# Optimization experiments

Hardware: AMD Instinct MI355X
Metric: run time of the kernel (lower is better)

## Reference

```python
import jax, jax.numpy as jnp
import numpy as np

NENV, SEQ, LATENT = 4096, 128, 64
EMB, HID = 256, 1024
SA = 2  # state_action_size


def setup_inputs() -> dict:
    key = jax.random.key(0)
    ks = jax.random.split(key, 8)
    def w(k, shape):
        return (jax.random.normal(k, shape, jnp.float32) / np.sqrt(shape[0])).astype(jnp.float32)
    return {
        "z": jax.random.normal(ks[0], (NENV, SEQ, LATENT), jnp.float32),
        "rnn_hxs": jnp.zeros((NENV, HID), jnp.float32),
        "w1": w(ks[1], (SA + LATENT, 32)), "b1": jnp.zeros((32,), jnp.float32),
        "w2": w(ks[2], (32, EMB)),          "b2": jnp.zeros((EMB,), jnp.float32),
        "wih": w(ks[3], (EMB, 3 * HID)),    "bih": jnp.zeros((3 * HID,), jnp.float32),
        "whh": w(ks[4], (HID, 3 * HID)),    "bhh": jnp.zeros((3 * HID,), jnp.float32),
        "w3": w(ks[5], (HID, HID // 2)),    "b3": jnp.zeros((HID // 2,), jnp.float32),
        "w4": w(ks[6], (HID // 2, SA)),     "b4": jnp.zeros((SA,), jnp.float32),
    }


def _gru_cell(x, h, wih, whh, bih, bhh):
    # PyTorch nn.GRU single-step semantics.
    gi = x @ wih + bih                    # [n, 3H]
    gh = h @ whh + bhh                    # [n, 3H]
    i_r, i_z, i_n = jnp.split(gi, 3, axis=-1)
    h_r, h_z, h_n = jnp.split(gh, 3, axis=-1)
    r = jax.nn.sigmoid(i_r + h_r)
    u = jax.nn.sigmoid(i_z + h_z)
    n = jnp.tanh(i_n + r * h_n)
    return (1.0 - u) * n + u * h


def reference(z, rnn_hxs, w1, b1, w2, b2, wih, bih, whh, bhh, w3, b3, w4, b4):
    zt = jnp.transpose(z, (1, 0, 2))                     # [S, N, latent]
    state0 = -2.0 * jnp.ones((z.shape[0], SA), z.dtype)  # initial fake action/state

    def step(carry, z_t):
        state, h = carry
        x = jnp.concatenate([state, z_t], axis=-1)       # [N, 2+latent]
        x = jax.nn.relu(x @ w1 + b1)
        x = jax.nn.relu(x @ w2 + b2)                     # mlp_in -> [N, EMB]
        h = _gru_cell(x, h, wih, whh, bih, bhh)          # [N, HID]
        o = jax.nn.relu(h @ w3 + b3)
        o = jnp.tanh(o @ w4 + b4)                        # output_linear -> [N, 2]
        return (o, h), o

    (_, h_new), outs = jax.lax.scan(step, (state0, rnn_hxs), zt)
    # original returns outputs.permute(1,0,2) -> [nenv, seq, 2], plus new hidden
    return jnp.transpose(outs, (1, 0, 2)), h_new
```

## Files before the change

kernel.cpp:

```cpp
#include <hip/hip_runtime.h>
#include <cstdint>
#include <cstddef>

#define NENV 4096
#define SEQ  128
#define LATENT 64
#define EMB  256
#define HID  1024
#define SA   2

typedef _Float16 half8 __attribute__((ext_vector_type(8)));
typedef float f32x4 __attribute__((ext_vector_type(4)));

__device__ __forceinline__ float sigmoid_f(float x){ return 1.0f/(1.0f + __expf(-x)); }

__global__ void transpose_cvt_kernel(const float* __restrict__ in, _Float16* __restrict__ out,
                                     int K, int C){
  int n = K*C;
  for (int i = blockIdx.x*blockDim.x + threadIdx.x; i < n; i += gridDim.x*blockDim.x){
    int c = i / K;
    int k = i - c*K;
    out[i] = (_Float16)in[(size_t)k*C + c];
  }
}

__global__ void init_h_kernel(const float* __restrict__ rnn, float* __restrict__ h32,
                              _Float16* __restrict__ h16){
  int n = NENV*HID;
  for (int i = blockIdx.x*blockDim.x + threadIdx.x; i < n; i += gridDim.x*blockDim.x){
    float v = rnn[i];
    h32[i] = v;
    h16[i] = (_Float16)v;
  }
}

__device__ __forceinline__ void gru_kloop(
    const _Float16* __restrict__ A, const _Float16* __restrict__ W, int K,
    int r0, int c0, int arow, int aseg, int m, int q, int n0,
    _Float16* As, _Float16* Ws0, _Float16* Ws1, _Float16* Ws2,
    f32x4* acc_r, f32x4* acc_z, f32x4* accn)
{
  for (int k0 = 0; k0 < K; k0 += 32){
    half8 la  = *(const half8*)(A + (size_t)(r0 + arow)*K + k0 + aseg*8);
    half8 lw0 = *(const half8*)(W + (size_t)(          c0 + arow)*K + k0 + aseg*8);
    half8 lw1 = *(const half8*)(W + (size_t)(HID     + c0 + arow)*K + k0 + aseg*8);
    half8 lw2 = *(const half8*)(W + (size_t)(2*HID   + c0 + arow)*K + k0 + aseg*8);
    __syncthreads();
    *(half8*)&As [arow*40 + aseg*8] = la;
    *(half8*)&Ws0[arow*40 + aseg*8] = lw0;
    *(half8*)&Ws1[arow*40 + aseg*8] = lw1;
    *(half8*)&Ws2[arow*40 + aseg*8] = lw2;
    __syncthreads();
    half8 br = *(const half8*)&Ws0[(n0+m)*40 + q*8];
    half8 bz = *(const half8*)&Ws1[(n0+m)*40 + q*8];
    half8 bn = *(const half8*)&Ws2[(n0+m)*40 + q*8];
#pragma unroll
    for (int mt = 0; mt < 4; ++mt){
      half8 a = *(const half8*)&As[(mt*16 + m)*40 + q*8];
      acc_r[mt] = __builtin_amdgcn_mfma_f32_16x16x32_f16(a, br, acc_r[mt], 0, 0, 0);
      acc_z[mt] = __builtin_amdgcn_mfma_f32_16x16x32_f16(a, bz, acc_z[mt], 0, 0, 0);
      accn[mt]  = __builtin_amdgcn_mfma_f32_16x16x32_f16(a, bn, accn[mt], 0, 0, 0);
    }
  }
}

__global__ __launch_bounds__(256, 4) void gru_kernel(
    const _Float16* __restrict__ x2h, const _Float16* __restrict__ hcur16,
    const _Float16* __restrict__ wihT, const _Float16* __restrict__ whhT,
    const float* __restrict__ bih, const float* __restrict__ bhh,
    float* __restrict__ h32, _Float16* __restrict__ hnxt16)
{
  __shared__ _Float16 As[64*40];
  __shared__ _Float16 Ws0[64*40];
  __shared__ _Float16 Ws1[64*40];
  __shared__ _Float16 Ws2[64*40];
  const int r0 = blockIdx.x*64, c0 = blockIdx.y*64;
  const int tid = threadIdx.x;
  const int lane = tid & 63, wave = tid >> 6;
  const int m = lane & 15, q = lane >> 4, n0 = wave*16;
  const int arow = tid >> 2, aseg = tid & 3;

  f32x4 zero4 = {0.f, 0.f, 0.f, 0.f};
  f32x4 acc_r[4], acc_z[4], acc_in[4], acc_hn[4];
#pragma unroll
  for (int i = 0; i < 4; ++i){ acc_r[i]=zero4; acc_z[i]=zero4; acc_in[i]=zero4; acc_hn[i]=zero4; }

  gru_kloop(x2h,    wihT, EMB, r0, c0, arow, aseg, m, q, n0, As, Ws0, Ws1, Ws2, acc_r, acc_z, acc_in);
  gru_kloop(hcur16, whhT, HID, r0, c0, arow, aseg, m, q, n0, As, Ws0, Ws1, Ws2, acc_r, acc_z, acc_hn);

  const int gc = c0 + n0 + m;
  float b_r  = bih[gc]         + bhh[gc];
  float b_z  = bih[gc + HID]   + bhh[gc + HID];
  float b_in = bih[gc + 2*HID];
  float b_hn = bhh[gc + 2*HID];
#pragma unroll
  for (int mt = 0; mt < 4; ++mt){
#pragma unroll
    for (int r = 0; r < 4; ++r){
      int grow = r0 + mt*16 + q*4 + r;
      float rr = sigmoid_f(acc_r[mt][r] + b_r);
      float u  = sigmoid_f(acc_z[mt][r] + b_z);
      float nn = tanhf(acc_in[mt][r] + b_in + rr*(acc_hn[mt][r] + b_hn));
      size_t idx = (size_t)grow*HID + gc;
      float hold = h32[idx];
      float hnew = (1.0f - u)*nn + u*hold;
      h32[idx] = hnew;
      hnxt16[idx] = (_Float16)hnew;
    }
  }
}

__global__ __launch_bounds__(256, 4) void out1_kernel(
    const _Float16* __restrict__ h16, const _Float16* __restrict__ w3T,
    const float* __restrict__ b3, float* __restrict__ o1)
{
  __shared__ _Float16 As[64*40];
  __shared__ _Float16 Ws[64*40];
  const int r0 = blockIdx.x*64, c0 = blockIdx.y*64;
  const int tid = threadIdx.x;
  const int lane = tid & 63, wave = tid >> 6;
  const int m = lane & 15, q = lane >> 4, n0 = wave*16;
  const int arow = tid >> 2, aseg = tid & 3;

  f32x4 zero4 = {0.f, 0.f, 0.f, 0.f};
  f32x4 acc[4];
#pragma unroll
  for (int i = 0; i < 4; ++i) acc[i] = zero4;

  for (int k0 = 0; k0 < HID; k0 += 32){
    half8 la = *(const half8*)(h16 + (size_t)(r0 + arow)*HID + k0 + aseg*8);
    half8 lw = *(const half8*)(w3T + (size_t)(c0 + arow)*HID + k0 + aseg*8);
    __syncthreads();
    *(half8*)&As[arow*40 + aseg*8] = la;
    *(half8*)&Ws[arow*40 + aseg*8] = lw;
    __syncthreads();
    half8 b = *(const half8*)&Ws[(n0+m)*40 + q*8];
#pragma unroll
    for (int mt = 0; mt < 4; ++mt){
      half8 a = *(const half8*)&As[(mt*16 + m)*40 + q*8];
      acc[mt] = __builtin_amdgcn_mfma_f32_16x16x32_f16(a, b, acc[mt], 0, 0, 0);
    }
  }
  const int gc = c0 + n0 + m;
  float bb = b3[gc];
#pragma unroll
  for (int mt = 0; mt < 4; ++mt){
#pragma unroll
    for (int r = 0; r < 4; ++r){
      int grow = r0 + mt*16 + q*4 + r;
      o1[(size_t)grow*(HID/2) + gc] = fmaxf(acc[mt][r] + bb, 0.f);
    }
  }
}

__global__ void tail_head_kernel(
    const float* __restrict__ o1, const float* __restrict__ w4, const float* __restrict__ b4,
    const float* __restrict__ z,  const float* __restrict__ w1, const float* __restrict__ b1,
    const float* __restrict__ w2, const float* __restrict__ b2,
    _Float16* __restrict__ x2h, float* __restrict__ out, int t, int mode)
{
  __shared__ float sw2[32*256];
  __shared__ float sw1[66*32];
  __shared__ float sz[16][64];
  __shared__ float sx1[16][32];
  __shared__ float sst[16][2];
  const int tid = threadIdx.x;
  const int r0 = blockIdx.x*16;

  if (mode != 2){
    for (int i = tid; i < 66*32; i += 256) sw1[i] = w1[i];
    for (int i = tid; i < 32*256; i += 256) sw2[i] = w2[i];
    int zt = (mode == 0) ? 0 : (t + 1);
    for (int i = tid; i < 16*64; i += 256){
      int r = i >> 6, k = i & 63;
      sz[r][k] = z[(size_t)(r0 + r)*SEQ*LATENT + zt*LATENT + k];
    }
  }

  if (mode != 0){
    int r = tid >> 4, p = tid & 15;
    const float* orow = o1 + (size_t)(r0 + r)*(HID/2);
    float a0 = 0.f, a1 = 0.f;
    for (int k = p*32; k < p*32 + 32; ++k){
      float v = orow[k];
      a0 += v*w4[k*2];
      a1 += v*w4[k*2 + 1];
    }
#pragma unroll
    for (int off = 1; off < 16; off <<= 1){
      a0 += __shfl_xor(a0, off);
      a1 += __shfl_xor(a1, off);
    }
    if (p == 0){
      a0 = tanhf(a0 + b4[0]);
      a1 = tanhf(a1 + b4[1]);
      out[(size_t)(r0 + r)*SEQ*SA + t*SA + 0] = a0;
      out[(size_t)(r0 + r)*SEQ*SA + t*SA + 1] = a1;
      sst[r][0] = a0; sst[r][1] = a1;
    }
  } else {
    if (tid < 32) sst[tid >> 1][tid & 1] = -2.0f;
  }
  __syncthreads();

  if (mode != 2){
    for (int it = tid; it < 16*32; it += 256){
      int r = it >> 5, j = it & 31;
      float acc = b1[j];
      acc += sst[r][0]*sw1[0*32 + j] + sst[r][1]*sw1[1*32 + j];
#pragma unroll 8
      for (int k = 0; k < 64; ++k) acc += sz[r][k]*sw1[(k + 2)*32 + j];
      sx1[r][j] = fmaxf(acc, 0.f);
    }
    __syncthreads();
    int col = tid;
    for (int r = 0; r < 16; ++r){
      float acc = b2[col];
#pragma unroll
      for (int k = 0; k < 32; ++k) acc += sx1[r][k]*sw2[k*256 + col];
      x2h[(size_t)(r0 + r)*EMB + col] = (_Float16)fmaxf(acc, 0.f);
    }
  }
}

extern "C" void kernel_launch(void* const* d_in, const int* in_sizes, int n_in,
                              void* d_out, int out_size, void* d_ws, size_t ws_size,
                              hipStream_t stream) {
  const float* z   = (const float*)d_in[0];
  const float* rnn = (const float*)d_in[1];
  const float* w1  = (const float*)d_in[2];
  const float* b1  = (const float*)d_in[3];
  const float* w2  = (const float*)d_in[4];
  const float* b2  = (const float*)d_in[5];
  const float* wih = (const float*)d_in[6];
  const float* bih = (const float*)d_in[7];
  const float* whh = (const float*)d_in[8];
  const float* bhh = (const float*)d_in[9];
  const float* w3  = (const float*)d_in[10];
  const float* b3  = (const float*)d_in[11];
  const float* w4  = (const float*)d_in[12];
  const float* b4  = (const float*)d_in[13];
  float* out = (float*)d_out;

  char* ws = (char*)d_ws;
  _Float16* wihT = (_Float16*)ws;                 ws += (size_t)3*HID*EMB*2;
  _Float16* whhT = (_Float16*)ws;                 ws += (size_t)3*HID*HID*2;
  _Float16* w3T  = (_Float16*)ws;                 ws += (size_t)(HID/2)*HID*2;
  _Float16* h16a = (_Float16*)ws;                 ws += (size_t)NENV*HID*2;
  _Float16* h16b = (_Float16*)ws;                 ws += (size_t)NENV*HID*2;
  float*    h32  = (float*)ws;                    ws += (size_t)NENV*HID*4;
  _Float16* x2h  = (_Float16*)ws;                 ws += (size_t)NENV*EMB*2;
  float*    o1   = (float*)ws;                    ws += (size_t)NENV*(HID/2)*4;

  transpose_cvt_kernel<<<512, 256, 0, stream>>>(wih, wihT, EMB, 3*HID);
  transpose_cvt_kernel<<<1024, 256, 0, stream>>>(whh, whhT, HID, 3*HID);
  transpose_cvt_kernel<<<256, 256, 0, stream>>>(w3, w3T, HID, HID/2);
  init_h_kernel<<<1024, 256, 0, stream>>>(rnn, h32, h16a);

  tail_head_kernel<<<NENV/16, 256, 0, stream>>>(o1, w4, b4, z, w1, b1, w2, b2, x2h, out, 0, 0);

  for (int t = 0; t < SEQ; ++t){
    _Float16* hc = (t & 1) ? h16b : h16a;
    _Float16* hn = (t & 1) ? h16a : h16b;
    gru_kernel<<<dim3(NENV/64, HID/64), 256, 0, stream>>>(x2h, hc, wihT, whhT, bih, bhh, h32, hn);
    out1_kernel<<<dim3(NENV/64, (HID/2)/64), 256, 0, stream>>>(hn, w3T, b3, o1);
    tail_head_kernel<<<NENV/16, 256, 0, stream>>>(o1, w4, b4, z, w1, b1, w2, b2, x2h, out,
                                                  t, (t < SEQ - 1) ? 1 : 2);
  }

  hipMemcpyAsync(out + (size_t)NENV*SEQ*SA, h32, (size_t)NENV*HID*sizeof(float),
                 hipMemcpyDeviceToDevice, stream);
}
```

Baseline: 11.20 ms.

## Retile GRU and output GEMMs to 128-row tiles with 32x32 MFMA and direct LDS loads

The GRU and out1 GEMM kernels now use 128x64 block tiles, 32x32x16 MFMA instructions, and global_load_lds DMA that writes straight into shared memory instead of going through registers. Block indices are remapped so neighbouring column groups land on the same XCD, which is meant to improve L2 reuse of weights. The o1 intermediate is stored in fp16 to halve its traffic. Together these aim to raise MFMA utilization and cut global and LDS traffic. The cost is fewer resident blocks per CU, an unpadded LDS layout that may cause bank conflicts, and reduced precision for o1.

Result: slower. 13.35 ms (+19.2%).

```diff
diff --git a/kernel.cpp b/kernel.cpp
--- a/kernel.cpp
+++ b/kernel.cpp
@@ -10,9 +10,19 @@
 #define SA   2
 
 typedef _Float16 half8 __attribute__((ext_vector_type(8)));
-typedef float f32x4 __attribute__((ext_vector_type(4)));
+typedef float f32x16 __attribute__((ext_vector_type(16)));
 
 __device__ __forceinline__ float sigmoid_f(float x){ return 1.0f/(1.0f + __expf(-x)); }
+
+__device__ __forceinline__ void dma16(const void* g, void* l){
+  __builtin_amdgcn_global_load_lds(
+      (const __attribute__((address_space(1))) void*)g,
+      (__attribute__((address_space(3))) void*)l, 16, 0, 0);
+}
+
+__device__ __forceinline__ f32x16 mfma32(half8 a, half8 b, f32x16 c){
+  return __builtin_amdgcn_mfma_f32_32x32x16_f16(a, b, c, 0, 0, 0);
+}
 
 __global__ void transpose_cvt_kernel(const float* __restrict__ in, _Float16* __restrict__ out,
                                      int K, int C){
@@ -34,127 +44,162 @@
   }
 }
 
-__device__ __forceinline__ void gru_kloop(
-    const _Float16* __restrict__ A, const _Float16* __restrict__ W, int K,
-    int r0, int c0, int arow, int aseg, int m, int q, int n0,
-    _Float16* As, _Float16* Ws0, _Float16* Ws1, _Float16* Ws2,
-    f32x4* acc_r, f32x4* acc_z, f32x4* accn)
+__device__ __forceinline__ void gru_phase(
+    const _Float16* __restrict__ Ap, const _Float16* __restrict__ Wp, int K,
+    int r0, int c0, int tid, int wave, int lane, int rbase, int cbase,
+    half8* smem, f32x16* accR, f32x16* accZ, f32x16* accN)
 {
+  const int l31 = lane & 31, lhi = lane >> 5;
+  const _Float16* g0; const _Float16* g1; const _Float16* g2; const _Float16* g3; const _Float16* g4;
+  { int slot = tid;        int kc = slot >> 7, row = slot & 127;
+    g0 = Ap + (size_t)(r0 + row)*K + kc*8; }
+  { int slot = 256 + tid;  int kc = slot >> 7, row = slot & 127;
+    g1 = Ap + (size_t)(r0 + row)*K + kc*8; }
+  { int s2 = tid;          int gate = s2 >> 8, kc = (s2 >> 6) & 3, col = s2 & 63;
+    g2 = Wp + (size_t)(gate*HID + c0 + col)*K + kc*8; }
+  { int s2 = 256 + tid;    int gate = s2 >> 8, kc = (s2 >> 6) & 3, col = s2 & 63;
+    g3 = Wp + (size_t)(gate*HID + c0 + col)*K + kc*8; }
+  { int s2 = 512 + tid;    int gate = s2 >> 8, kc = (s2 >> 6) & 3, col = s2 & 63;
+    g4 = Wp + (size_t)(gate*HID + c0 + col)*K + kc*8; }
+  char* lbase = (char*)smem;
+  char* l0 = lbase + (size_t)(0*256 + wave*64)*16;
+  char* l1 = lbase + (size_t)(1*256 + wave*64)*16;
+  char* l2 = lbase + (size_t)(2*256 + wave*64)*16;
+  char* l3 = lbase + (size_t)(3*256 + wave*64)*16;
+  char* l4 = lbase + (size_t)(4*256 + wave*64)*16;
+
   for (int k0 = 0; k0 < K; k0 += 32){
-    half8 la  = *(const half8*)(A + (size_t)(r0 + arow)*K + k0 + aseg*8);
-    half8 lw0 = *(const half8*)(W + (size_t)(          c0 + arow)*K + k0 + aseg*8);
-    half8 lw1 = *(const half8*)(W + (size_t)(HID     + c0 + arow)*K + k0 + aseg*8);
-    half8 lw2 = *(const half8*)(W + (size_t)(2*HID   + c0 + arow)*K + k0 + aseg*8);
-    __syncthreads();
-    *(half8*)&As [arow*40 + aseg*8] = la;
-    *(half8*)&Ws0[arow*40 + aseg*8] = lw0;
-    *(half8*)&Ws1[arow*40 + aseg*8] = lw1;
-    *(half8*)&Ws2[arow*40 + aseg*8] = lw2;
-    __syncthreads();
-    half8 br = *(const half8*)&Ws0[(n0+m)*40 + q*8];
-    half8 bz = *(const half8*)&Ws1[(n0+m)*40 + q*8];
-    half8 bn = *(const half8*)&Ws2[(n0+m)*40 + q*8];
-#pragma unroll
-    for (int mt = 0; mt < 4; ++mt){
-      half8 a = *(const half8*)&As[(mt*16 + m)*40 + q*8];
-      acc_r[mt] = __builtin_amdgcn_mfma_f32_16x16x32_f16(a, br, acc_r[mt], 0, 0, 0);
-      acc_z[mt] = __builtin_amdgcn_mfma_f32_16x16x32_f16(a, bz, acc_z[mt], 0, 0, 0);
-      accn[mt]  = __builtin_amdgcn_mfma_f32_16x16x32_f16(a, bn, accn[mt], 0, 0, 0);
-    }
-  }
-}
-
-__global__ __launch_bounds__(256, 4) void gru_kernel(
-    const _Float16* __restrict__ x2h, const _Float16* __restrict__ hcur16,
+    dma16(g0, l0); dma16(g1, l1); dma16(g2, l2); dma16(g3, l3); dma16(g4, l4);
+    g0 += 32; g1 += 32; g2 += 32; g3 += 32; g4 += 32;
+    __syncthreads();
+#pragma unroll
+    for (int c = 0; c < 2; ++c){
+      const int kc = c*2 + lhi;
+      half8 a0 = smem[kc*128 + rbase      + l31];
+      half8 a1 = smem[kc*128 + rbase + 32 + l31];
+      half8 b0 = smem[512 +        kc*64 + cbase + l31];
+      half8 b1 = smem[512 + 256 +  kc*64 + cbase + l31];
+      half8 b2 = smem[512 + 512 +  kc*64 + cbase + l31];
+      accR[0] = mfma32(a0, b0, accR[0]);
+      accR[1] = mfma32(a1, b0, accR[1]);
+      accZ[0] = mfma32(a0, b1, accZ[0]);
+      accZ[1] = mfma32(a1, b1, accZ[1]);
+      accN[0] = mfma32(a0, b2, accN[0]);
+      accN[1] = mfma32(a1, b2, accN[1]);
+    }
+    __syncthreads();
+  }
+}
+
+__global__ __launch_bounds__(256, 2) void gru_kernel(
+    const _Float16* __restrict__ x2h, const _Float16* __restrict__ hcur,
     const _Float16* __restrict__ wihT, const _Float16* __restrict__ whhT,
     const float* __restrict__ bih, const float* __restrict__ bhh,
-    float* __restrict__ h32, _Float16* __restrict__ hnxt16)
+    float* __restrict__ h32, _Float16* __restrict__ hnxt)
 {
-  __shared__ _Float16 As[64*40];
-  __shared__ _Float16 Ws0[64*40];
-  __shared__ _Float16 Ws1[64*40];
-  __shared__ _Float16 Ws2[64*40];
-  const int r0 = blockIdx.x*64, c0 = blockIdx.y*64;
+  __shared__ half8 smem[1280];
   const int tid = threadIdx.x;
   const int lane = tid & 63, wave = tid >> 6;
-  const int m = lane & 15, q = lane >> 4, n0 = wave*16;
-  const int arow = tid >> 2, aseg = tid & 3;
-
-  f32x4 zero4 = {0.f, 0.f, 0.f, 0.f};
-  f32x4 acc_r[4], acc_z[4], acc_in[4], acc_hn[4];
-#pragma unroll
-  for (int i = 0; i < 4; ++i){ acc_r[i]=zero4; acc_z[i]=zero4; acc_in[i]=zero4; acc_hn[i]=zero4; }
-
-  gru_kloop(x2h,    wihT, EMB, r0, c0, arow, aseg, m, q, n0, As, Ws0, Ws1, Ws2, acc_r, acc_z, acc_in);
-  gru_kloop(hcur16, whhT, HID, r0, c0, arow, aseg, m, q, n0, As, Ws0, Ws1, Ws2, acc_r, acc_z, acc_hn);
-
-  const int gc = c0 + n0 + m;
-  float b_r  = bih[gc]         + bhh[gc];
-  float b_z  = bih[gc + HID]   + bhh[gc + HID];
-  float b_in = bih[gc + 2*HID];
-  float b_hn = bhh[gc + 2*HID];
-#pragma unroll
-  for (int mt = 0; mt < 4; ++mt){
-#pragma unroll
-    for (int r = 0; r < 4; ++r){
-      int grow = r0 + mt*16 + q*4 + r;
-      float rr = sigmoid_f(acc_r[mt][r] + b_r);
-      float u  = sigmoid_f(acc_z[mt][r] + b_z);
-      float nn = tanhf(acc_in[mt][r] + b_in + rr*(acc_hn[mt][r] + b_hn));
-      size_t idx = (size_t)grow*HID + gc;
+  const int id = blockIdx.x;
+  const int xcd = id & 7, slot = id >> 3;
+  const int colg = xcd*2 + (slot & 1);
+  const int rowg = slot >> 1;
+  const int r0 = rowg*128, c0 = colg*64;
+  const int rbase = (wave & 1)*64, cbase = (wave >> 1)*32;
+  const int l31 = lane & 31, lhi = lane >> 5;
+
+  f32x16 accR[2], accZ[2], accN1[2], accN2[2];
+#pragma unroll
+  for (int i = 0; i < 16; ++i){
+    accR[0][i]=0.f; accR[1][i]=0.f; accZ[0][i]=0.f; accZ[1][i]=0.f;
+    accN1[0][i]=0.f; accN1[1][i]=0.f; accN2[0][i]=0.f; accN2[1][i]=0.f;
+  }
+
+  gru_phase(x2h,  wihT, EMB, r0, c0, tid, wave, lane, rbase, cbase, smem, accR, accZ, accN1);
+  gru_phase(hcur, whhT, HID, r0, c0, tid, wave, lane, rbase, cbase, smem, accR, accZ, accN2);
+
+  const int gc = c0 + cbase + l31;
+  const float b_r  = bih[gc]         + bhh[gc];
+  const float b_z  = bih[gc + HID]   + bhh[gc + HID];
+  const float b_in = bih[gc + 2*HID];
+  const float b_hn = bhh[gc + 2*HID];
+#pragma unroll
+  for (int rt = 0; rt < 2; ++rt){
+#pragma unroll
+    for (int reg = 0; reg < 16; ++reg){
+      int row = r0 + rbase + rt*32 + (reg & 3) + 8*(reg >> 2) + 4*lhi;
+      float rr = sigmoid_f(accR[rt][reg] + b_r);
+      float u  = sigmoid_f(accZ[rt][reg] + b_z);
+      float nn = tanhf(accN1[rt][reg] + b_in + rr*(accN2[rt][reg] + b_hn));
+      size_t idx = (size_t)row*HID + gc;
       float hold = h32[idx];
       float hnew = (1.0f - u)*nn + u*hold;
       h32[idx] = hnew;
-      hnxt16[idx] = (_Float16)hnew;
-    }
-  }
-}
-
-__global__ __launch_bounds__(256, 4) void out1_kernel(
+      hnxt[idx] = (_Float16)hnew;
+    }
+  }
+}
+
+__global__ __launch_bounds__(256, 2) void out1_kernel(
     const _Float16* __restrict__ h16, const _Float16* __restrict__ w3T,
-    const float* __restrict__ b3, float* __restrict__ o1)
+    const float* __restrict__ b3, _Float16* __restrict__ o1)
 {
-  __shared__ _Float16 As[64*40];
-  __shared__ _Float16 Ws[64*40];
-  const int r0 = blockIdx.x*64, c0 = blockIdx.y*64;
+  __shared__ half8 smem[768];
   const int tid = threadIdx.x;
   const int lane = tid & 63, wave = tid >> 6;
-  const int m = lane & 15, q = lane >> 4, n0 = wave*16;
-  const int arow = tid >> 2, aseg = tid & 3;
-
-  f32x4 zero4 = {0.f, 0.f, 0.f, 0.f};
-  f32x4 acc[4];
-#pragma unroll
-  for (int i = 0; i < 4; ++i) acc[i] = zero4;
+  const int id = blockIdx.x;
+  const int colg = id & 7;
+  const int rowg = id >> 3;
+  const int r0 = rowg*128, c0 = colg*64;
+  const int rbase = (wave & 1)*64, cbase = (wave >> 1)*32;
+  const int l31 = lane & 31, lhi = lane >> 5;
+
+  f32x16 acc[2];
+#pragma unroll
+  for (int i = 0; i < 16; ++i){ acc[0][i]=0.f; acc[1][i]=0.f; }
+
+  const _Float16* g0; const _Float16* g1; const _Float16* g2;
+  { int slot = tid;       int kc = slot >> 7, row = slot & 127;
+    g0 = h16 + (size_t)(r0 + row)*HID + kc*8; }
+  { int slot = 256 + tid; int kc = slot >> 7, row = slot & 127;
+    g1 = h16 + (size_t)(r0 + row)*HID + kc*8; }
+  { int kc = tid >> 6, col = tid & 63;
+    g2 = w3T + (size_t)(c0 + col)*HID + kc*8; }
+  char* lbase = (char*)smem;
+  char* l0 = lbase + (size_t)(0*256 + wave*64)*16;
+  char* l1 = lbase + (size_t)(1*256 + wave*64)*16;
+  char* l2 = lbase + (size_t)(2*256 + wave*64)*16;
 
   for (int k0 = 0; k0 < HID; k0 += 32){
-    half8 la = *(const half8*)(h16 + (size_t)(r0 + arow)*HID + k0 + aseg*8);
-    half8 lw = *(const half8*)(w3T + (size_t)(c0 + arow)*HID + k0 + aseg*8);
-    __syncthreads();
-    *(half8*)&As[arow*40 + aseg*8] = la;
-    *(half8*)&Ws[arow*40 + aseg*8] = lw;
-    __syncthreads();
-    half8 b = *(const half8*)&Ws[(n0+m)*40 + q*8];
-#pragma unroll
-    for (int mt = 0; mt < 4; ++mt){
-      half8 a = *(const half8*)&As[(mt*16 + m)*40 + q*8];
-      acc[mt] = __builtin_amdgcn_mfma_f32_16x16x32_f16(a, b, acc[mt], 0, 0, 0);
-    }
-  }
-  const int gc = c0 + n0 + m;
-  float bb = b3[gc];
-#pragma unroll
-  for (int mt = 0; mt < 4; ++mt){
-#pragma unroll
-    for (int r = 0; r < 4; ++r){
-      int grow = r0 + mt*16 + q*4 + r;
-      o1[(size_t)grow*(HID/2) + gc] = fmaxf(acc[mt][r] + bb, 0.f);
+    dma16(g0, l0); dma16(g1, l1); dma16(g2, l2);
+    g0 += 32; g1 += 32; g2 += 32;
+    __syncthreads();
+#pragma unroll
+    for (int c = 0; c < 2; ++c){
+      const int kc = c*2 + lhi;
+      half8 a0 = smem[kc*128 + rbase      + l31];
+      half8 a1 = smem[kc*128 + rbase + 32 + l31];
+      half8 b  = smem[512 + kc*64 + cbase + l31];
+      acc[0] = mfma32(a0, b, acc[0]);
+      acc[1] = mfma32(a1, b, acc[1]);
+    }
+    __syncthreads();
+  }
+
+  const int gc = c0 + cbase + l31;
+  const float bb = b3[gc];
+#pragma unroll
+  for (int rt = 0; rt < 2; ++rt){
+#pragma unroll
+    for (int reg = 0; reg < 16; ++reg){
+      int row = r0 + rbase + rt*32 + (reg & 3) + 8*(reg >> 2) + 4*lhi;
+      o1[(size_t)row*(HID/2) + gc] = (_Float16)fmaxf(acc[rt][reg] + bb, 0.f);
     }
   }
 }
 
 __global__ void tail_head_kernel(
-    const float* __restrict__ o1, const float* __restrict__ w4, const float* __restrict__ b4,
+    const _Float16* __restrict__ o1, const float* __restrict__ w4, const float* __restrict__ b4,
     const float* __restrict__ z,  const float* __restrict__ w1, const float* __restrict__ b1,
     const float* __restrict__ w2, const float* __restrict__ b2,
     _Float16* __restrict__ x2h, float* __restrict__ out, int t, int mode)
@@ -179,10 +224,10 @@
 
   if (mode != 0){
     int r = tid >> 4, p = tid & 15;
-    const float* orow = o1 + (size_t)(r0 + r)*(HID/2);
+    const _Float16* orow = o1 + (size_t)(r0 + r)*(HID/2);
     float a0 = 0.f, a1 = 0.f;
     for (int k = p*32; k < p*32 + 32; ++k){
-      float v = orow[k];
+      float v = (float)orow[k];
       a0 += v*w4[k*2];
       a1 += v*w4[k*2 + 1];
     }
@@ -250,7 +295,7 @@
   _Float16* h16b = (_Float16*)ws;                 ws += (size_t)NENV*HID*2;
   float*    h32  = (float*)ws;                    ws += (size_t)NENV*HID*4;
   _Float16* x2h  = (_Float16*)ws;                 ws += (size_t)NENV*EMB*2;
-  float*    o1   = (float*)ws;                    ws += (size_t)NENV*(HID/2)*4;
+  _Float16* o1   = (_Float16*)ws;                 ws += (size_t)NENV*(HID/2)*2;
 
   transpose_cvt_kernel<<<512, 256, 0, stream>>>(wih, wihT, EMB, 3*HID);
   transpose_cvt_kernel<<<1024, 256, 0, stream>>>(whh, whhT, HID, 3*HID);
@@ -262,8 +307,8 @@
   for (int t = 0; t < SEQ; ++t){
     _Float16* hc = (t & 1) ? h16b : h16a;
     _Float16* hn = (t & 1) ? h16a : h16b;
-    gru_kernel<<<dim3(NENV/64, HID/64), 256, 0, stream>>>(x2h, hc, wihT, whhT, bih, bhh, h32, hn);
-    out1_kernel<<<dim3(NENV/64, (HID/2)/64), 256, 0, stream>>>(hn, w3T, b3, o1);
+    gru_kernel<<<512, 256, 0, stream>>>(x2h, hc, wihT, whhT, bih, bhh, h32, hn);
+    out1_kernel<<<256, 256, 0, stream>>>(hn, w3T, b3, o1);
     tail_head_kernel<<<NENV/16, 256, 0, stream>>>(o1, w4, b4, z, w1, b1, w2, b2, x2h, out,
                                                   t, (t < SEQ - 1) ? 1 : 2);
   }
```

## Use direct global-to-LDS loads, drop fp32 hidden state, fp16 intermediate output

Applied to the files above, without the earlier changes.

The GEMM kernels now stage tiles through global_load_lds DMA straight into unpadded LDS instead of going through registers. The fp32 hidden-state copy is removed: the recurrence reads the old h from the fp16 buffer and writes fp32 only on the final step, and the o1 activations are stored as fp16. Block ids are remapped so that neighbouring blocks share weight column groups. Together these cut global traffic and register staging, but carrying h in fp16 across 128 steps may hurt accuracy, and the unpadded LDS layout may cause bank conflicts.

Result: faster. 10.90 ms (-2.7%).

```diff
diff --git a/kernel.cpp b/kernel.cpp
--- a/kernel.cpp
+++ b/kernel.cpp
@@ -13,6 +13,16 @@
 typedef float f32x4 __attribute__((ext_vector_type(4)));
 
 __device__ __forceinline__ float sigmoid_f(float x){ return 1.0f/(1.0f + __expf(-x)); }
+
+__device__ __forceinline__ void dma16(const void* g, void* l){
+  __builtin_amdgcn_global_load_lds(
+      (const __attribute__((address_space(1))) void*)g,
+      (__attribute__((address_space(3))) void*)l, 16, 0, 0);
+}
+
+__device__ __forceinline__ f32x4 mfma16(half8 a, half8 b, f32x4 c){
+  return __builtin_amdgcn_mfma_f32_16x16x32_f16(a, b, c, 0, 0, 0);
+}
 
 __global__ void transpose_cvt_kernel(const float* __restrict__ in, _Float16* __restrict__ out,
                                      int K, int C){
@@ -24,137 +34,149 @@
   }
 }
 
-__global__ void init_h_kernel(const float* __restrict__ rnn, float* __restrict__ h32,
-                              _Float16* __restrict__ h16){
+__global__ void init_h_kernel(const float* __restrict__ rnn, _Float16* __restrict__ h16){
   int n = NENV*HID;
   for (int i = blockIdx.x*blockDim.x + threadIdx.x; i < n; i += gridDim.x*blockDim.x){
-    float v = rnn[i];
-    h32[i] = v;
-    h16[i] = (_Float16)v;
-  }
-}
-
-__device__ __forceinline__ void gru_kloop(
-    const _Float16* __restrict__ A, const _Float16* __restrict__ W, int K,
-    int r0, int c0, int arow, int aseg, int m, int q, int n0,
-    _Float16* As, _Float16* Ws0, _Float16* Ws1, _Float16* Ws2,
-    f32x4* acc_r, f32x4* acc_z, f32x4* accn)
-{
-  for (int k0 = 0; k0 < K; k0 += 32){
-    half8 la  = *(const half8*)(A + (size_t)(r0 + arow)*K + k0 + aseg*8);
-    half8 lw0 = *(const half8*)(W + (size_t)(          c0 + arow)*K + k0 + aseg*8);
-    half8 lw1 = *(const half8*)(W + (size_t)(HID     + c0 + arow)*K + k0 + aseg*8);
-    half8 lw2 = *(const half8*)(W + (size_t)(2*HID   + c0 + arow)*K + k0 + aseg*8);
-    __syncthreads();
-    *(half8*)&As [arow*40 + aseg*8] = la;
-    *(half8*)&Ws0[arow*40 + aseg*8] = lw0;
-    *(half8*)&Ws1[arow*40 + aseg*8] = lw1;
-    *(half8*)&Ws2[arow*40 + aseg*8] = lw2;
-    __syncthreads();
-    half8 br = *(const half8*)&Ws0[(n0+m)*40 + q*8];
-    half8 bz = *(const half8*)&Ws1[(n0+m)*40 + q*8];
-    half8 bn = *(const half8*)&Ws2[(n0+m)*40 + q*8];
-#pragma unroll
-    for (int mt = 0; mt < 4; ++mt){
-      half8 a = *(const half8*)&As[(mt*16 + m)*40 + q*8];
-      acc_r[mt] = __builtin_amdgcn_mfma_f32_16x16x32_f16(a, br, acc_r[mt], 0, 0, 0);
-      acc_z[mt] = __builtin_amdgcn_mfma_f32_16x16x32_f16(a, bz, acc_z[mt], 0, 0, 0);
-      accn[mt]  = __builtin_amdgcn_mfma_f32_16x16x32_f16(a, bn, accn[mt], 0, 0, 0);
-    }
+    h16[i] = (_Float16)rnn[i];
   }
 }
 
 __global__ __launch_bounds__(256, 4) void gru_kernel(
-    const _Float16* __restrict__ x2h, const _Float16* __restrict__ hcur16,
+    const _Float16* __restrict__ x2h, const _Float16* __restrict__ hcur,
     const _Float16* __restrict__ wihT, const _Float16* __restrict__ whhT,
     const float* __restrict__ bih, const float* __restrict__ bhh,
-    float* __restrict__ h32, _Float16* __restrict__ hnxt16)
+    _Float16* __restrict__ hnxt, float* __restrict__ hout)
 {
-  __shared__ _Float16 As[64*40];
-  __shared__ _Float16 Ws0[64*40];
-  __shared__ _Float16 Ws1[64*40];
-  __shared__ _Float16 Ws2[64*40];
-  const int r0 = blockIdx.x*64, c0 = blockIdx.y*64;
+  __shared__ half8 sA[256];
+  __shared__ half8 sB[3][256];
   const int tid = threadIdx.x;
   const int lane = tid & 63, wave = tid >> 6;
   const int m = lane & 15, q = lane >> 4, n0 = wave*16;
-  const int arow = tid >> 2, aseg = tid & 3;
-
-  f32x4 zero4 = {0.f, 0.f, 0.f, 0.f};
-  f32x4 acc_r[4], acc_z[4], acc_in[4], acc_hn[4];
-#pragma unroll
-  for (int i = 0; i < 4; ++i){ acc_r[i]=zero4; acc_z[i]=zero4; acc_in[i]=zero4; acc_hn[i]=zero4; }
-
-  gru_kloop(x2h,    wihT, EMB, r0, c0, arow, aseg, m, q, n0, As, Ws0, Ws1, Ws2, acc_r, acc_z, acc_in);
-  gru_kloop(hcur16, whhT, HID, r0, c0, arow, aseg, m, q, n0, As, Ws0, Ws1, Ws2, acc_r, acc_z, acc_hn);
+  const int row = tid >> 2, seg = tid & 3;
+
+  const int id = blockIdx.x;
+  const int colg = (id & 7)*2 + ((id >> 3) & 1);
+  const int rowg = id >> 4;
+  const int r0 = rowg*64, c0 = colg*64;
+
+  f32x4 accR[4], accZ[4], accNi[4], accNh[4];
+#pragma unroll
+  for (int i = 0; i < 4; ++i){
+    accR[i] = (f32x4){0.f,0.f,0.f,0.f};
+    accZ[i] = (f32x4){0.f,0.f,0.f,0.f};
+    accNi[i] = (f32x4){0.f,0.f,0.f,0.f};
+    accNh[i] = (f32x4){0.f,0.f,0.f,0.f};
+  }
+
+  char* dA  = (char*)&sA[wave*64];
+  char* dB0 = (char*)&sB[0][wave*64];
+  char* dB1 = (char*)&sB[1][wave*64];
+  char* dB2 = (char*)&sB[2][wave*64];
+
+#pragma unroll
+  for (int phase = 0; phase < 2; ++phase){
+    const _Float16* A = phase ? hcur : x2h;
+    const _Float16* W = phase ? whhT : wihT;
+    const int K = phase ? HID : EMB;
+    f32x4* accN = phase ? accNh : accNi;
+
+    const _Float16* gA  = A + (size_t)(r0 + row)*K + seg*8;
+    const _Float16* gB0 = W + (size_t)(0*HID + c0 + row)*K + seg*8;
+    const _Float16* gB1 = W + (size_t)(1*HID + c0 + row)*K + seg*8;
+    const _Float16* gB2 = W + (size_t)(2*HID + c0 + row)*K + seg*8;
+
+    for (int k0 = 0; k0 < K; k0 += 32){
+      dma16(gA, dA); dma16(gB0, dB0); dma16(gB1, dB1); dma16(gB2, dB2);
+      gA += 32; gB0 += 32; gB1 += 32; gB2 += 32;
+      __syncthreads();
+      half8 b0 = sB[0][(n0+m)*4 + q];
+      half8 b1 = sB[1][(n0+m)*4 + q];
+      half8 b2 = sB[2][(n0+m)*4 + q];
+#pragma unroll
+      for (int mt = 0; mt < 4; ++mt){
+        half8 a = sA[(mt*16 + m)*4 + q];
+        accR[mt] = mfma16(a, b0, accR[mt]);
+        accZ[mt] = mfma16(a, b1, accZ[mt]);
+        accN[mt] = mfma16(a, b2, accN[mt]);
+      }
+      __syncthreads();
+    }
+  }
 
   const int gc = c0 + n0 + m;
-  float b_r  = bih[gc]         + bhh[gc];
-  float b_z  = bih[gc + HID]   + bhh[gc + HID];
-  float b_in = bih[gc + 2*HID];
-  float b_hn = bhh[gc + 2*HID];
+  const float b_r  = bih[gc]         + bhh[gc];
+  const float b_z  = bih[gc + HID]   + bhh[gc + HID];
+  const float b_in = bih[gc + 2*HID];
+  const float b_hn = bhh[gc + 2*HID];
 #pragma unroll
   for (int mt = 0; mt < 4; ++mt){
 #pragma unroll
     for (int r = 0; r < 4; ++r){
       int grow = r0 + mt*16 + q*4 + r;
-      float rr = sigmoid_f(acc_r[mt][r] + b_r);
-      float u  = sigmoid_f(acc_z[mt][r] + b_z);
-      float nn = tanhf(acc_in[mt][r] + b_in + rr*(acc_hn[mt][r] + b_hn));
+      float rr = sigmoid_f(accR[mt][r] + b_r);
+      float u  = sigmoid_f(accZ[mt][r] + b_z);
+      float nn = tanhf(accNi[mt][r] + b_in + rr*(accNh[mt][r] + b_hn));
       size_t idx = (size_t)grow*HID + gc;
-      float hold = h32[idx];
+      float hold = (float)hcur[idx];
       float hnew = (1.0f - u)*nn + u*hold;
-      h32[idx] = hnew;
-      hnxt16[idx] = (_Float16)hnew;
+      hnxt[idx] = (_Float16)hnew;
+      if (hout) hout[idx] = hnew;
     }
   }
 }
 
 __global__ __launch_bounds__(256, 4) void out1_kernel(
     const _Float16* __restrict__ h16, const _Float16* __restrict__ w3T,
-    const float* __restrict__ b3, float* __restrict__ o1)
+    const float* __restrict__ b3, _Float16* __restrict__ o1)
 {
-  __shared__ _Float16 As[64*40];
-  __shared__ _Float16 Ws[64*40];
-  const int r0 = blockIdx.x*64, c0 = blockIdx.y*64;
+  __shared__ half8 sA[256];
+  __shared__ half8 sB[256];
   const int tid = threadIdx.x;
   const int lane = tid & 63, wave = tid >> 6;
   const int m = lane & 15, q = lane >> 4, n0 = wave*16;
-  const int arow = tid >> 2, aseg = tid & 3;
-
-  f32x4 zero4 = {0.f, 0.f, 0.f, 0.f};
+  const int row = tid >> 2, seg = tid & 3;
+
+  const int id = blockIdx.x;
+  const int colg = id & 7;
+  const int rowg = id >> 3;
+  const int r0 = rowg*64, c0 = colg*64;
+
   f32x4 acc[4];
 #pragma unroll
-  for (int i = 0; i < 4; ++i) acc[i] = zero4;
+  for (int i = 0; i < 4; ++i) acc[i] = (f32x4){0.f,0.f,0.f,0.f};
+
+  char* dA = (char*)&sA[wave*64];
+  char* dB = (char*)&sB[wave*64];
+  const _Float16* gA = h16 + (size_t)(r0 + row)*HID + seg*8;
+  const _Float16* gB = w3T + (size_t)(c0 + row)*HID + seg*8;
 
   for (int k0 = 0; k0 < HID; k0 += 32){
-    half8 la = *(const half8*)(h16 + (size_t)(r0 + arow)*HID + k0 + aseg*8);
-    half8 lw = *(const half8*)(w3T + (size_t)(c0 + arow)*HID + k0 + aseg*8);
+    dma16(gA, dA); dma16(gB, dB);
+    gA += 32; gB += 32;
     __syncthreads();
-    *(half8*)&As[arow*40 + aseg*8] = la;
-    *(half8*)&Ws[arow*40 + aseg*8] = lw;
+    half8 b = sB[(n0+m)*4 + q];
+#pragma unroll
+    for (int mt = 0; mt < 4; ++mt){
+      half8 a = sA[(mt*16 + m)*4 + q];
+      acc[mt] = mfma16(a, b, acc[mt]);
+    }
     __syncthreads();
-    half8 b = *(const half8*)&Ws[(n0+m)*40 + q*8];
-#pragma unroll
-    for (int mt = 0; mt < 4; ++mt){
-      half8 a = *(const half8*)&As[(mt*16 + m)*40 + q*8];
-      acc[mt] = __builtin_amdgcn_mfma_f32_16x16x32_f16(a, b, acc[mt], 0, 0, 0);
-    }
-  }
+  }
+
   const int gc = c0 + n0 + m;
-  float bb = b3[gc];
+  const float bb = b3[gc];
 #pragma unroll
   for (int mt = 0; mt < 4; ++mt){
 #pragma unroll
     for (int r = 0; r < 4; ++r){
       int grow = r0 + mt*16 + q*4 + r;
-      o1[(size_t)grow*(HID/2) + gc] = fmaxf(acc[mt][r] + bb, 0.f);
+      o1[(size_t)grow*(HID/2) + gc] = (_Float16)fmaxf(acc[mt][r] + bb, 0.f);
     }
   }
 }
 
 __global__ void tail_head_kernel(
-    const float* __restrict__ o1, const float* __restrict__ w4, const float* __restrict__ b4,
+    const _Float16* __restrict__ o1, const float* __restrict__ w4, const float* __restrict__ b4,
     const float* __restrict__ z,  const float* __restrict__ w1, const float* __restrict__ b1,
     const float* __restrict__ w2, const float* __restrict__ b2,
     _Float16* __restrict__ x2h, float* __restrict__ out, int t, int mode)
@@ -179,10 +201,10 @@
 
   if (mode != 0){
     int r = tid >> 4, p = tid & 15;
-    const float* orow = o1 + (size_t)(r0 + r)*(HID/2);
+    const _Float16* orow = o1 + (size_t)(r0 + r)*(HID/2);
     float a0 = 0.f, a1 = 0.f;
     for (int k = p*32; k < p*32 + 32; ++k){
-      float v = orow[k];
+      float v = (float)orow[k];
       a0 += v*w4[k*2];
       a1 += v*w4[k*2 + 1];
     }
@@ -248,26 +270,24 @@
   _Float16* w3T  = (_Float16*)ws;                 ws += (size_t)(HID/2)*HID*2;
   _Float16* h16a = (_Float16*)ws;                 ws += (size_t)NENV*HID*2;
   _Float16* h16b = (_Float16*)ws;                 ws += (size_t)NENV*HID*2;
-  float*    h32  = (float*)ws;                    ws += (size_t)NENV*HID*4;
   _Float16* x2h  = (_Float16*)ws;                 ws += (size_t)NENV*EMB*2;
-  float*    o1   = (float*)ws;                    ws += (size_t)NENV*(HID/2)*4;
+  _Float16* o1   = (_Float16*)ws;                 ws += (size_t)NENV*(HID/2)*2;
 
   transpose_cvt_kernel<<<512, 256, 0, stream>>>(wih, wihT, EMB, 3*HID);
   transpose_cvt_kernel<<<1024, 256, 0, stream>>>(whh, whhT, HID, 3*HID);
   transpose_cvt_kernel<<<256, 256, 0, stream>>>(w3, w3T, HID, HID/2);
-  init_h_kernel<<<1024, 256, 0, stream>>>(rnn, h32, h16a);
+  init_h_kernel<<<1024, 256, 0, stream>>>(rnn, h16a);
 
   tail_head_kernel<<<NENV/16, 256, 0, stream>>>(o1, w4, b4, z, w1, b1, w2, b2, x2h, out, 0, 0);
 
+  float* hfinal = out + (size_t)NENV*SEQ*SA;
   for (int t = 0; t < SEQ; ++t){
     _Float16* hc = (t & 1) ? h16b : h16a;
     _Float16* hn = (t & 1) ? h16a : h16b;
-    gru_kernel<<<dim3(NENV/64, HID/64), 256, 0, stream>>>(x2h, hc, wihT, whhT, bih, bhh, h32, hn);
-    out1_kernel<<<dim3(NENV/64, (HID/2)/64), 256, 0, stream>>>(hn, w3T, b3, o1);
+    gru_kernel<<<1024, 256, 0, stream>>>(x2h, hc, wihT, whhT, bih, bhh, hn,
+                                         (t == SEQ - 1) ? hfinal : nullptr);
+    out1_kernel<<<512, 256, 0, stream>>>(hn, w3T, b3, o1);
     tail_head_kernel<<<NENV/16, 256, 0, stream>>>(o1, w4, b4, z, w1, b1, w2, b2, x2h, out,
                                                   t, (t < SEQ - 1) ? 1 : 2);
   }
-
-  hipMemcpyAsync(out + (size_t)NENV*SEQ*SA, h32, (size_t)NENV*HID*sizeof(float),
-                 hipMemcpyDeviceToDevice, stream);
-}
+}
```
